# Kernel optimization log

Measured on AMD Instinct MI355X. Metric: run time of the kernel, lower is better.

## Reference

```python
import jax, jax.numpy as jnp
import numpy as np

N = 20000   # num_eeg_channels (graph nodes)
T = 512     # num_eeg_timesteps (GIN in_channels)
L = 256     # latent_features
HID = 512   # GIN hidden_channels
H = 4       # GATv2 heads
D = L // H  # per-head dim = 64
E = 320000  # edges


def setup_inputs() -> dict:
    key = jax.random.key(0)
    ks = jax.random.split(key, 16)
    s = 0.02
    f32 = jnp.float32
    return {
        "x": jax.random.normal(ks[0], (N, T), f32),
        "edge_index": jax.random.randint(ks[1], (2, E), 0, N, dtype=jnp.int64),
        "edge_attr": jax.random.normal(ks[2], (E,), f32),
        # GIN layer 1 MLP [T->HID->HID]
        "W1a": jax.random.normal(ks[3], (T, HID), f32) * s, "b1a": jnp.zeros((HID,), f32),
        "W1b": jax.random.normal(ks[4], (HID, HID), f32) * s, "b1b": jnp.zeros((HID,), f32),
        # GIN layer 2 MLP [HID->L->L]
        "W2a": jax.random.normal(ks[5], (HID, L), f32) * s, "b2a": jnp.zeros((L,), f32),
        "W2b": jax.random.normal(ks[6], (L, L), f32) * s, "b2b": jnp.zeros((L,), f32),
        # BatchNorm1d(L)
        "bn_g": jnp.ones((L,), f32), "bn_b": jnp.zeros((L,), f32),
        # GATv2Conv(L -> D, heads=H), separate src/dst projections, att vec, bias
        "Wl": jax.random.normal(ks[7], (L, H * D), f32) * s,
        "Wr": jax.random.normal(ks[8], (L, H * D), f32) * s,
        "att": jax.random.normal(ks[9], (H, D), f32) * s,
        "gat_b": jnp.zeros((H * D,), f32),
        # LayerNorm(N*L) and Linear(N*L, 1)
        "ln_g": jnp.ones((N * L,), f32), "ln_b": jnp.zeros((N * L,), f32),
        "Wp": jax.random.normal(ks[10], (N * L, 1), f32) * 0.001, "bp": jnp.zeros((1,), f32),
    }


def reference(x, edge_index, edge_attr, W1a, b1a, W1b, b1b, W2a, b2a, W2b, b2b,
              bn_g, bn_b, Wl, Wr, att, gat_b, ln_g, ln_b, Wp, bp):
    src, dst = edge_index[0], edge_index[1]

    # ---- GIN (2 layers; GINConv eps=0, edge_attr unused by GINConv) ----
    def gin_conv(h, Wa, ba, Wb, bb):
        agg = jax.ops.segment_sum(h[src], dst, num_segments=N)  # sum_{j->i} h_j
        z = h + agg
        return jax.nn.relu(z @ Wa + ba) @ Wb + bb

    h = jax.nn.relu(gin_conv(x, W1a, b1a, W1b, b1b))  # inter-layer ReLU
    h = gin_conv(h, W2a, b2a, W2b, b2b)               # [N, L]

    # ---- BatchNorm1d over node batch (training stats, biased var) ----
    mu = h.mean(axis=0)
    var = ((h - mu) ** 2).mean(axis=0)
    h = (h - mu) / jnp.sqrt(var + 1e-5) * bn_g + bn_b

    # ---- GATv2Conv (add_self_loops=False, eval so no attn dropout) ----
    xl = (h @ Wl).reshape(N, H, D)
    xr = (h @ Wr).reshape(N, H, D)
    e = jnp.einsum('ehd,hd->eh', jax.nn.leaky_relu(xl[src] + xr[dst], 0.2), att)  # [E,H]
    m = jax.ops.segment_max(e, dst, num_segments=N)          # per-target max
    ex = jnp.exp(e - m[dst])
    alpha = ex / jax.ops.segment_sum(ex, dst, num_segments=N)[dst]  # [E,H]
    gat_out = jax.ops.segment_sum(alpha[:, :, None] * xl[src], dst, num_segments=N)
    gat_out = gat_out.reshape(N, H * D) + gat_b              # [N, L]

    # ---- edge-attention scatter-add to nodes (faithful .view(4,-1)) ----
    edge_w = alpha.reshape(H, -1)                            # [H, E] (row-major, as torch .view)
    flat_idx = jnp.concatenate([src, dst])                   # each edge hits both endpoints
    vals = jnp.concatenate([edge_w, edge_w], axis=1)         # [H, 2E]
    node_att = jnp.zeros((H, N), e.dtype).at[:, flat_idx].add(vals)
    deg = jnp.bincount(edge_index.reshape(-1), length=N).astype(e.dtype)
    node_att = jax.nn.softmax(node_att / (deg + 1e-9)[None, :], axis=1)

    # ---- LayerNorm(N*L) + Linear + sigmoid ----
    feat = gat_out.reshape(1, N * L)
    fmu = feat.mean()
    fvar = ((feat - fmu) ** 2).mean()
    feat = (feat - fmu) / jnp.sqrt(fvar + 1e-5) * ln_g + ln_b
    pred = jax.nn.sigmoid(feat @ Wp + bp)                    # [1,1]

    return pred, node_att.mean(axis=0), edge_w.mean(axis=0)
```

## Files before the change

### kernel.cpp

```cpp
#include <hip/hip_runtime.h>
#include <hip/hip_bf16.h>

#define NN 20000
#define TT 512
#define LL 256
#define HH 4
#define DD 64
#define EE 320000

typedef __attribute__((ext_vector_type(8))) short short8;
typedef __attribute__((ext_vector_type(4))) float f32x4;

__device__ __forceinline__ float bf2f(unsigned short u) {
    return __uint_as_float((unsigned)u << 16);
}
__device__ __forceinline__ unsigned short f2bf(float f) {
    __hip_bfloat16 h = __float2bfloat16(f);
    unsigned short r;
    __builtin_memcpy(&r, &h, 2);
    return r;
}

__global__ void deg_kernel(const int* __restrict__ src, const int* __restrict__ dst,
                           int* deg_in, int* deg_tot) {
    int e = blockIdx.x * blockDim.x + threadIdx.x;
    if (e >= EE) return;
    atomicAdd(&deg_in[dst[e]], 1);
    atomicAdd(&deg_tot[src[e]], 1);
    atomicAdd(&deg_tot[dst[e]], 1);
}

__global__ void scan2_kernel(const int* __restrict__ deg0, int* rs0,
                             const int* __restrict__ deg1, int* rs1, int n) {
    __shared__ int sm[1024];
    __shared__ int s_carry;
    const int* deg = (blockIdx.x == 0) ? deg0 : deg1;
    int* row_start = (blockIdx.x == 0) ? rs0 : rs1;
    int tid = threadIdx.x;
    if (tid == 0) s_carry = 0;
    __syncthreads();
    for (int base = 0; base < n; base += 1024) {
        int i = base + tid;
        int v = (i < n) ? deg[i] : 0;
        sm[tid] = v;
        __syncthreads();
        for (int off = 1; off < 1024; off <<= 1) {
            int t = (tid >= off) ? sm[tid - off] : 0;
            __syncthreads();
            sm[tid] += t;
            __syncthreads();
        }
        int incl = sm[tid];
        int carry = s_carry;
        if (i < n) row_start[i] = carry + incl - v;
        __syncthreads();
        if (tid == 1023) s_carry = carry + sm[1023];
        __syncthreads();
    }
    if (tid == 0) row_start[n] = s_carry;
}

__global__ void fill_csr_kernel(const int* __restrict__ dst, const int* __restrict__ row_start,
                                int* cursor, int* csr) {
    int e = blockIdx.x * blockDim.x + threadIdx.x;
    if (e >= EE) return;
    int d = dst[e];
    int p = atomicAdd(&cursor[d], 1);
    csr[row_start[d] + p] = e;
}

__global__ void fill_adj2_kernel(const int* __restrict__ src, const int* __restrict__ dst,
                                 const int* __restrict__ rs2, int* cursor2, int* adj2) {
    int e = blockIdx.x * blockDim.x + threadIdx.x;
    if (e >= EE) return;
    int s = src[e];
    int p = atomicAdd(&cursor2[s], 1);
    adj2[rs2[s] + p] = e;
    int t = dst[e];
    int q = atomicAdd(&cursor2[t], 1);
    adj2[rs2[t] + q] = e;
}

__global__ void cast_bf_kernel(const float* __restrict__ in, unsigned short* __restrict__ out,
                               int n4) {
    int i = blockIdx.x * blockDim.x + threadIdx.x;
    if (i >= n4) return;
    float4 v = ((const float4*)in)[i];
    ushort4 o;
    o.x = f2bf(v.x); o.y = f2bf(v.y); o.z = f2bf(v.z); o.w = f2bf(v.w);
    ((ushort4*)out)[i] = o;
}

__global__ void wtrans_kernel(const float* __restrict__ W, unsigned short* __restrict__ Wt,
                              int K, int N) {
    __shared__ float t[32][33];
    int x = threadIdx.x & 31, y = threadIdx.x >> 5;
    int bn = blockIdx.x * 32, bk = blockIdx.y * 32;
#pragma unroll
    for (int i = 0; i < 32; i += 8) t[y + i][x] = W[(size_t)(bk + y + i) * N + bn + x];
    __syncthreads();
#pragma unroll
    for (int i = 0; i < 32; i += 8)
        Wt[(size_t)(bn + y + i) * K + bk + x] = f2bf(t[x][y + i]);
}

__global__ void agg_add_bf_kernel(const unsigned short* __restrict__ X,
                                  unsigned short* __restrict__ Z,
                                  const int* __restrict__ csr, const int* __restrict__ row_start,
                                  const int* __restrict__ src) {
    __shared__ int s_src[256];
    const int node = blockIdx.x, tid = threadIdx.x;
    const unsigned int* Xu = (const unsigned int*)X;
    const int start = row_start[node], end = row_start[node + 1];
    unsigned int self = Xu[(size_t)node * 256 + tid];
    float a0 = bf2f((unsigned short)(self & 0xffff));
    float a1 = bf2f((unsigned short)(self >> 16));
    for (int k0 = start; k0 < end; k0 += 256) {
        int k = k0 + tid;
        if (k < end) s_src[tid] = src[csr[k]];
        __syncthreads();
        int cnt = min(256, end - k0);
        for (int j = 0; j < cnt; ++j) {
            unsigned int v = Xu[(size_t)s_src[j] * 256 + tid];
            a0 += bf2f((unsigned short)(v & 0xffff));
            a1 += bf2f((unsigned short)(v >> 16));
        }
        __syncthreads();
    }
    ((unsigned int*)Z)[(size_t)node * 256 + tid] =
        (unsigned int)f2bf(a0) | ((unsigned int)f2bf(a1) << 16);
}

template <int RELU, int OUT_BF16>
__global__ __launch_bounds__(256)
void gemm_mfma_kernel(const unsigned short* __restrict__ A,
                      const unsigned short* __restrict__ Bt,
                      const float* __restrict__ bias, void* __restrict__ Cout,
                      int M, int K, int Nn) {
    __shared__ unsigned short lds[2][2][4][128][8];
    const int tid = threadIdx.x;
    const int wid = tid >> 6, lane = tid & 63;
    const int brow = blockIdx.y * 128, bcol = blockIdx.x * 128;
    const int wr = wid >> 1, wc = wid & 1;
    const int khi = lane >> 4, r15 = lane & 15;

    f32x4 acc[4][4] = {};

    const int q0 = wid * 2, q1 = wid * 2 + 1;
    const int kh0 = q0 >> 1, rh0 = q0 & 1;
    const int kh1 = q1 >> 1, rh1 = q1 & 1;
    int ar0 = brow + rh0 * 64 + lane; ar0 = ar0 < M ? ar0 : M - 1;
    int ar1 = brow + rh1 * 64 + lane; ar1 = ar1 < M ? ar1 : M - 1;
    const int bc0 = bcol + rh0 * 64 + lane;
    const int bc1 = bcol + rh1 * 64 + lane;
    const unsigned short* gA0 = A + (size_t)ar0 * K + kh0 * 8;
    const unsigned short* gA1 = A + (size_t)ar1 * K + kh1 * 8;
    const unsigned short* gB0 = Bt + (size_t)bc0 * K + kh0 * 8;
    const unsigned short* gB1 = Bt + (size_t)bc1 * K + kh1 * 8;

#define GLL(gp, lp) __builtin_amdgcn_global_load_lds( \
        (const __attribute__((address_space(1))) unsigned int*)(gp), \
        (__attribute__((address_space(3))) unsigned int*)(lp), 16, 0, 0)
#define STAGE(buf, kt) do { const int koff = (kt) * 32; \
        GLL(gA0 + koff, &lds[buf][0][kh0][rh0 * 64][0]); \
        GLL(gA1 + koff, &lds[buf][0][kh1][rh1 * 64][0]); \
        GLL(gB0 + koff, &lds[buf][1][kh0][rh0 * 64][0]); \
        GLL(gB1 + koff, &lds[buf][1][kh1][rh1 * 64][0]); \
    } while (0)

    const int NT = K >> 5;
    STAGE(0, 0);
    for (int kt = 0; kt < NT; ++kt) {
        const int cur = kt & 1;
        __syncthreads();
        if (kt + 1 < NT) STAGE(cur ^ 1, kt + 1);
        short8 af[4], bfv[4];
#pragma unroll
        for (int m = 0; m < 4; ++m)
            af[m] = *(const short8*)&lds[cur][0][khi][wr * 64 + m * 16 + r15][0];
#pragma unroll
        for (int n = 0; n < 4; ++n)
            bfv[n] = *(const short8*)&lds[cur][1][khi][wc * 64 + n * 16 + r15][0];
#pragma unroll
        for (int m = 0; m < 4; ++m)
#pragma unroll
            for (int n = 0; n < 4; ++n)
                acc[m][n] =
                    __builtin_amdgcn_mfma_f32_16x16x32_bf16(af[m], bfv[n], acc[m][n], 0, 0, 0);
    }
#undef STAGE
#undef GLL

#pragma unroll
    for (int m = 0; m < 4; ++m) {
#pragma unroll
        for (int n = 0; n < 4; ++n) {
            const int col = bcol + wc * 64 + n * 16 + r15;
            const float bb = bias ? bias[col] : 0.f;
            f32x4 v = acc[m][n];
#pragma unroll
            for (int r = 0; r < 4; ++r) {
                const int row = brow + wr * 64 + m * 16 + khi * 4 + r;
                if (row < M) {
                    float o = v[r] + bb;
                    if (RELU) o = fmaxf(o, 0.f);
                    if (OUT_BF16)
                        ((unsigned short*)Cout)[(size_t)row * Nn + col] = f2bf(o);
                    else
                        ((float*)Cout)[(size_t)row * Nn + col] = o;
                }
            }
        }
    }
}

__global__ void bn_stats_kernel(const float* __restrict__ h, float* cs, float* csq) {
    int col = threadIdx.x;
    int r0 = blockIdx.x * 100;
    int r1 = min(r0 + 100, NN);
    float s = 0.f, sq = 0.f;
    for (int r = r0; r < r1; r++) {
        float v = h[(size_t)r * 256 + col];
        s += v;
        sq += v * v;
    }
    atomicAdd(&cs[col], s);
    atomicAdd(&csq[col], sq);
}

__global__ void bn_apply_bf_kernel(const float* __restrict__ h, const float* __restrict__ cs,
                                   const float* __restrict__ csq, const float* __restrict__ g,
                                   const float* __restrict__ b, unsigned short* __restrict__ out) {
    int i = blockIdx.x * blockDim.x + threadIdx.x;
    if (i >= NN * 256) return;
    int col = i & 255;
    float mu = cs[col] * (1.f / NN);
    float var = csq[col] * (1.f / NN) - mu * mu;
    float inv = rsqrtf(var + 1e-5f);
    out[i] = f2bf((h[i] - mu) * inv * g[col] + b[col]);
}

__global__ void gat_fused_kernel(const unsigned short* __restrict__ xl,
                                 const unsigned short* __restrict__ xr,
                                 const int* __restrict__ csr, const int* __restrict__ rs,
                                 const int* __restrict__ src, const float* __restrict__ att,
                                 const float* __restrict__ gatb,
                                 float* __restrict__ alpha, float* __restrict__ out) {
    const int lane = threadIdx.x & 63;
    const int wave = threadIdx.x >> 6;
    const int node = blockIdx.x * 4 + wave;
    if (node >= NN) return;
    const int start = rs[node], end = rs[node + 1];
    const int deg = end - start;
    const int h = lane >> 4;
    const int l15 = lane & 15;

    const float4 attv = ((const float4*)att)[lane];
    const uint2 uxr = ((const uint2*)(xr + (size_t)node * 256))[lane];
    const float xr0 = bf2f((unsigned short)(uxr.x & 0xffff));
    const float xr1 = bf2f((unsigned short)(uxr.x >> 16));
    const float xr2 = bf2f((unsigned short)(uxr.y & 0xffff));
    const float xr3 = bf2f((unsigned short)(uxr.y >> 16));

    float m = -1e30f, S = 0.f;
    float O0 = 0.f, O1 = 0.f, O2 = 0.f, O3 = 0.f;
    float lg0 = 0.f, lg1 = 0.f, lg2 = 0.f, lg3 = 0.f;
    const bool fast = (deg <= 64);
    int eid = 0;

    for (int base = start; base < end; base += 64) {
        const int cnt = min(64, end - base);
        eid = (lane < cnt) ? csr[base + lane] : 0;
        int sid = (lane < cnt) ? src[eid] : 0;
        for (int i = 0; i < cnt; ++i) {
            const int s = __shfl(sid, i);
            const uint2 u = ((const uint2*)(xl + (size_t)s * 256))[lane];
            const float x0 = bf2f((unsigned short)(u.x & 0xffff));
            const float x1 = bf2f((unsigned short)(u.x >> 16));
            const float x2 = bf2f((unsigned short)(u.y & 0xffff));
            const float x3 = bf2f((unsigned short)(u.y >> 16));
            float a0 = x0 + xr0; a0 = a0 > 0.f ? a0 : 0.2f * a0;
            float a1 = x1 + xr1; a1 = a1 > 0.f ? a1 : 0.2f * a1;
            float a2 = x2 + xr2; a2 = a2 > 0.f ? a2 : 0.2f * a2;
            float a3 = x3 + xr3; a3 = a3 > 0.f ? a3 : 0.2f * a3;
            float p = a0 * attv.x + a1 * attv.y + a2 * attv.z + a3 * attv.w;
#pragma unroll
            for (int o = 1; o < 16; o <<= 1) p += __shfl_xor(p, o);
            if (fast && l15 == (i & 15)) {
                const int t = i >> 4;
                if (t == 0) lg0 = p;
                else if (t == 1) lg1 = p;
                else if (t == 2) lg2 = p;
                else lg3 = p;
            }
            const float mn = fmaxf(m, p);
            const float sc = __expf(m - mn);
            const float w = __expf(p - mn);
            S = S * sc + w;
            O0 = O0 * sc + w * x0;
            O1 = O1 * sc + w * x1;
            O2 = O2 * sc + w * x2;
            O3 = O3 * sc + w * x3;
            m = mn;
        }
    }

    const float rS = (deg > 0) ? 1.f / S : 0.f;
    const float4 bv = ((const float4*)gatb)[lane];
    float4 ov;
    ov.x = O0 * rS + bv.x; ov.y = O1 * rS + bv.y;
    ov.z = O2 * rS + bv.z; ov.w = O3 * rS + bv.w;
    ((float4*)(out + (size_t)node * 256))[lane] = ov;

    if (deg == 0) return;
    if (fast) {
#pragma unroll
        for (int t = 0; t < 4; ++t) {
            const int k = l15 + t * 16;
            if (k < deg) {
                const int e = __shfl(eid, k);
                const float l = (t == 0) ? lg0 : (t == 1) ? lg1 : (t == 2) ? lg2 : lg3;
                alpha[(size_t)e * 4 + h] = __expf(l - m) * rS;
            }
        }
    } else {
        for (int base = start; base < end; base += 64) {
            const int cnt = min(64, end - base);
            const int eid2 = (lane < cnt) ? csr[base + lane] : 0;
            const int sid2 = (lane < cnt) ? src[eid2] : 0;
            for (int i = 0; i < cnt; ++i) {
                const int s = __shfl(sid2, i);
                const uint2 u = ((const uint2*)(xl + (size_t)s * 256))[lane];
                float a0 = bf2f((unsigned short)(u.x & 0xffff)) + xr0; a0 = a0 > 0.f ? a0 : 0.2f * a0;
                float a1 = bf2f((unsigned short)(u.x >> 16)) + xr1;    a1 = a1 > 0.f ? a1 : 0.2f * a1;
                float a2 = bf2f((unsigned short)(u.y & 0xffff)) + xr2; a2 = a2 > 0.f ? a2 : 0.2f * a2;
                float a3 = bf2f((unsigned short)(u.y >> 16)) + xr3;    a3 = a3 > 0.f ? a3 : 0.2f * a3;
                float p = a0 * attv.x + a1 * attv.y + a2 * attv.z + a3 * attv.w;
#pragma unroll
                for (int o = 1; o < 16; o <<= 1) p += __shfl_xor(p, o);
                const int e = __shfl(eid2, i);
                if (l15 == 0) alpha[(size_t)e * 4 + h] = __expf(p - m) * rS;
            }
        }
    }
}

__global__ void node_att_gather_kernel(const float* __restrict__ abuf,
                                       const int* __restrict__ adj2,
                                       const int* __restrict__ rs2, float* __restrict__ na) {
    int lane = threadIdx.x & 63;
    int wave = threadIdx.x >> 6;
    int node = blockIdx.x * 4 + wave;
    if (node >= NN) return;
    int start = rs2[node], end = rs2[node + 1];
    float s0 = 0.f, s1 = 0.f, s2 = 0.f, s3 = 0.f;
    for (int k = start + lane; k < end; k += 64) {
        int e = adj2[k];
        s0 += abuf[e];
        s1 += abuf[EE + e];
        s2 += abuf[2 * EE + e];
        s3 += abuf[3 * EE + e];
    }
#pragma unroll
    for (int o = 32; o > 0; o >>= 1) {
        s0 += __shfl_xor(s0, o);
        s1 += __shfl_xor(s1, o);
        s2 += __shfl_xor(s2, o);
        s3 += __shfl_xor(s3, o);
    }
    if (lane == 0) {
        na[node] = s0;
        na[NN + node] = s1;
        na[2 * NN + node] = s2;
        na[3 * NN + node] = s3;
    }
}

__global__ void edge_mean_kernel(const float* __restrict__ abuf, float* __restrict__ out_edge) {
    int e = blockIdx.x * blockDim.x + threadIdx.x;
    if (e >= EE) return;
    out_edge[e] = 0.25f * (abuf[e] + abuf[EE + e] + abuf[2 * EE + e] + abuf[3 * EE + e]);
}

__global__ void head_stats_kernel(const float* __restrict__ na, const int* __restrict__ deg_tot,
                                  float* hm, float* hs) {
    __shared__ float red[1024];
    int h = blockIdx.x;
    int tid = threadIdx.x;
    float m = -1e30f;
    for (int i = tid; i < NN; i += 1024) {
        float v = na[h * NN + i] / ((float)deg_tot[i] + 1e-9f);
        m = fmaxf(m, v);
    }
    red[tid] = m;
    __syncthreads();
    for (int o = 512; o > 0; o >>= 1) {
        if (tid < o) red[tid] = fmaxf(red[tid], red[tid + o]);
        __syncthreads();
    }
    m = red[0];
    __syncthreads();
    float s = 0.f;
    for (int i = tid; i < NN; i += 1024) {
        float v = na[h * NN + i] / ((float)deg_tot[i] + 1e-9f);
        s += __expf(v - m);
    }
    red[tid] = s;
    __syncthreads();
    for (int o = 512; o > 0; o >>= 1) {
        if (tid < o) red[tid] += red[tid + o];
        __syncthreads();
    }
    if (tid == 0) {
        hm[h] = m;
        hs[h] = red[0];
    }
}

__global__ void node_out_kernel(const float* __restrict__ na, const int* __restrict__ deg_tot,
                                const float* __restrict__ hm, const float* __restrict__ hs,
                                float* __restrict__ out_node) {
    int i = blockIdx.x * blockDim.x + threadIdx.x;
    if (i >= NN) return;
    float acc = 0.f;
#pragma unroll
    for (int h = 0; h < 4; h++) {
        float v = na[h * NN + i] / ((float)deg_tot[i] + 1e-9f);
        acc += __expf(v - hm[h]) / hs[h];
    }
    out_node[i] = 0.25f * acc;
}

__global__ void ln_fused_kernel(const float* __restrict__ x, const float* __restrict__ g,
                                const float* __restrict__ b, const float* __restrict__ Wp,
                                float* __restrict__ part) {
    const int total4 = NN * 64;
    const float4* x4 = (const float4*)x;
    const float4* g4 = (const float4*)g;
    const float4* b4 = (const float4*)b;
    const float4* w4 = (const float4*)Wp;
    float s1 = 0.f, s2 = 0.f, s3 = 0.f, s4 = 0.f, s5 = 0.f;
    for (int i = blockIdx.x * blockDim.x + threadIdx.x; i < total4;
         i += gridDim.x * blockDim.x) {
        float4 xv = x4[i], gv = g4[i], bv = b4[i], wv = w4[i];
        s1 += xv.x + xv.y + xv.z + xv.w;
        s2 += xv.x * xv.x + xv.y * xv.y + xv.z * xv.z + xv.w * xv.w;
        float gw0 = gv.x * wv.x, gw1 = gv.y * wv.y, gw2 = gv.z * wv.z, gw3 = gv.w * wv.w;
        s3 += xv.x * gw0 + xv.y * gw1 + xv.z * gw2 + xv.w * gw3;
        s4 += gw0 + gw1 + gw2 + gw3;
        s5 += bv.x * wv.x + bv.y * wv.y + bv.z * wv.z + bv.w * wv.w;
    }
#pragma unroll
    for (int o = 32; o > 0; o >>= 1) {
        s1 += __shfl_xor(s1, o);
        s2 += __shfl_xor(s2, o);
        s3 += __shfl_xor(s3, o);
        s4 += __shfl_xor(s4, o);
        s5 += __shfl_xor(s5, o);
    }
    __shared__ float sm[4][5];
    int lane = threadIdx.x & 63, wv_ = threadIdx.x >> 6;
    if (lane == 0) {
        sm[wv_][0] = s1; sm[wv_][1] = s2; sm[wv_][2] = s3; sm[wv_][3] = s4; sm[wv_][4] = s5;
    }
    __syncthreads();
    if (threadIdx.x == 0) {
        float t1 = 0.f, t2 = 0.f, t3 = 0.f, t4 = 0.f, t5 = 0.f;
#pragma unroll
        for (int w = 0; w < 4; ++w) {
            t1 += sm[w][0]; t2 += sm[w][1]; t3 += sm[w][2]; t4 += sm[w][3]; t5 += sm[w][4];
        }
        part[0 * 512 + blockIdx.x] = t1;
        part[1 * 512 + blockIdx.x] = t2;
        part[2 * 512 + blockIdx.x] = t3;
        part[3 * 512 + blockIdx.x] = t4;
        part[4 * 512 + blockIdx.x] = t5;
    }
}

__global__ void ln_final_kernel(const float* __restrict__ part, const float* __restrict__ bp,
                                float* __restrict__ out) {
    float v0 = part[0 * 512 + threadIdx.x];
    float v1 = part[1 * 512 + threadIdx.x];
    float v2 = part[2 * 512 + threadIdx.x];
    float v3 = part[3 * 512 + threadIdx.x];
    float v4 = part[4 * 512 + threadIdx.x];
#pragma unroll
    for (int o = 32; o > 0; o >>= 1) {
        v0 += __shfl_xor(v0, o);
        v1 += __shfl_xor(v1, o);
        v2 += __shfl_xor(v2, o);
        v3 += __shfl_xor(v3, o);
        v4 += __shfl_xor(v4, o);
    }
    __shared__ float sm[8][5];
    int lane = threadIdx.x & 63, wv_ = threadIdx.x >> 6;
    if (lane == 0) {
        sm[wv_][0] = v0; sm[wv_][1] = v1; sm[wv_][2] = v2; sm[wv_][3] = v3; sm[wv_][4] = v4;
    }
    __syncthreads();
    if (threadIdx.x == 0) {
        float S1 = 0.f, S2 = 0.f, S3 = 0.f, S4 = 0.f, S5 = 0.f;
#pragma unroll
        for (int w = 0; w < 8; ++w) {
            S1 += sm[w][0]; S2 += sm[w][1]; S3 += sm[w][2]; S4 += sm[w][3]; S5 += sm[w][4];
        }
        const float M = (float)NN * 256.f;
        float mu = S1 / M;
        float var = S2 / M - mu * mu;
        float inv = rsqrtf(var + 1e-5f);
        float z = inv * (S3 - mu * S4) + S5 + bp[0];
        out[0] = 1.f / (1.f + __expf(-z));
    }
}

extern "C" void kernel_launch(void* const* d_in, const int* in_sizes, int n_in,
                              void* d_out, int out_size, void* d_ws, size_t ws_size,
                              hipStream_t stream) {
    const float* x    = (const float*)d_in[0];
    const int* ei     = (const int*)d_in[1];
    const float* W1a  = (const float*)d_in[3];
    const float* b1a  = (const float*)d_in[4];
    const float* W1b  = (const float*)d_in[5];
    const float* b1b  = (const float*)d_in[6];
    const float* W2a  = (const float*)d_in[7];
    const float* b2a  = (const float*)d_in[8];
    const float* W2b  = (const float*)d_in[9];
    const float* b2b  = (const float*)d_in[10];
    const float* bn_g = (const float*)d_in[11];
    const float* bn_b = (const float*)d_in[12];
    const float* Wl   = (const float*)d_in[13];
    const float* Wr   = (const float*)d_in[14];
    const float* att  = (const float*)d_in[15];
    const float* gatb = (const float*)d_in[16];
    const float* ln_g = (const float*)d_in[17];
    const float* ln_b = (const float*)d_in[18];
    const float* Wp   = (const float*)d_in[19];
    const float* bp   = (const float*)d_in[20];

    const int* src = ei;
    const int* dst = ei + EE;

    float* out = (float*)d_out;
    float* out_pred = out;
    float* out_node = out + 1;
    float* out_edge = out + 1 + NN;

    unsigned short* B0 = (unsigned short*)d_ws;
    unsigned short* B1 = B0 + (size_t)NN * 512;
    unsigned short* B2 = B1 + (size_t)NN * 512;
    unsigned short* B3 = B2 + (size_t)NN * 512;
    float* hbuf = (float*)B0;
    unsigned short* xl = B1;
    unsigned short* xr = B3;
    float* gout = (float*)B0;

    unsigned short* W1at = B3 + (size_t)NN * 512;
    unsigned short* W1bt = W1at + 512 * 512;
    unsigned short* W2at = W1bt + 512 * 512;
    unsigned short* W2bt = W2at + 256 * 512;
    unsigned short* Wlt  = W2bt + 256 * 256;
    unsigned short* Wrt  = Wlt + 256 * 256;
    float* alpha = (float*)(Wrt + 256 * 256);
    float* na    = alpha + (size_t)EE * 4;
    float* csum  = na + 4 * NN;
    float* csq_  = csum + 256;
    float* hm    = csq_ + 256;
    float* hs    = hm + 4;
    float* part  = hs + 4;
    int* deg_in     = (int*)(part + 5 * 512);
    int* deg_tot    = deg_in + NN;
    int* row_start  = deg_tot + NN;
    int* row_start2 = row_start + NN + 1;
    int* cursor     = row_start2 + NN + 1;
    int* cursor2    = cursor + NN;
    int* csr        = cursor2 + NN;
    int* adj2       = csr + EE;

    hipMemsetAsync(csum, 0, (size_t)(256 + 256 + 4 + 4) * sizeof(float), stream);
    hipMemsetAsync(deg_in, 0, (size_t)(6 * NN + 2) * sizeof(int), stream);

    const int EB = (EE + 255) / 256;

    wtrans_kernel<<<dim3(16, 16), 256, 0, stream>>>(W1a, W1at, 512, 512);
    wtrans_kernel<<<dim3(16, 16), 256, 0, stream>>>(W1b, W1bt, 512, 512);
    wtrans_kernel<<<dim3(8, 16), 256, 0, stream>>>(W2a, W2at, 512, 256);
    wtrans_kernel<<<dim3(8, 8), 256, 0, stream>>>(W2b, W2bt, 256, 256);
    wtrans_kernel<<<dim3(8, 8), 256, 0, stream>>>(Wl, Wlt, 256, 256);
    wtrans_kernel<<<dim3(8, 8), 256, 0, stream>>>(Wr, Wrt, 256, 256);

    cast_bf_kernel<<<(NN * 512 / 4 + 255) / 256, 256, 0, stream>>>(x, B0, NN * 512 / 4);

    deg_kernel<<<EB, 256, 0, stream>>>(src, dst, deg_in, deg_tot);
    scan2_kernel<<<2, 1024, 0, stream>>>(deg_in, row_start, deg_tot, row_start2, NN);
    fill_csr_kernel<<<EB, 256, 0, stream>>>(dst, row_start, cursor, csr);
    fill_adj2_kernel<<<EB, 256, 0, stream>>>(src, dst, row_start2, cursor2, adj2);

    agg_add_bf_kernel<<<NN, 256, 0, stream>>>(B0, B1, csr, row_start, src);
    gemm_mfma_kernel<1, 1><<<dim3(4, 157), 256, 0, stream>>>(B1, W1at, b1a, B2, NN, 512, 512);
    gemm_mfma_kernel<1, 1><<<dim3(4, 157), 256, 0, stream>>>(B2, W1bt, b1b, B3, NN, 512, 512);
    agg_add_bf_kernel<<<NN, 256, 0, stream>>>(B3, B0, csr, row_start, src);
    gemm_mfma_kernel<1, 1><<<dim3(2, 157), 256, 0, stream>>>(B0, W2at, b2a, B1, NN, 512, 256);
    gemm_mfma_kernel<0, 0><<<dim3(2, 157), 256, 0, stream>>>(B1, W2bt, b2b, hbuf, NN, 256, 256);

    bn_stats_kernel<<<200, 256, 0, stream>>>(hbuf, csum, csq_);
    bn_apply_bf_kernel<<<(NN * 256 + 255) / 256, 256, 0, stream>>>(hbuf, csum, csq_, bn_g, bn_b,
                                                                   B2);

    gemm_mfma_kernel<0, 1><<<dim3(2, 157), 256, 0, stream>>>(B2, Wlt, nullptr, xl, NN, 256, 256);
    gemm_mfma_kernel<0, 1><<<dim3(2, 157), 256, 0, stream>>>(B2, Wrt, nullptr, xr, NN, 256, 256);

    gat_fused_kernel<<<(NN + 3) / 4, 256, 0, stream>>>(xl, xr, csr, row_start, src, att, gatb,
                                                       alpha, gout);

    node_att_gather_kernel<<<NN / 4, 256, 0, stream>>>(alpha, adj2, row_start2, na);
    edge_mean_kernel<<<EB, 256, 0, stream>>>(alpha, out_edge);
    head_stats_kernel<<<4, 1024, 0, stream>>>(na, deg_tot, hm, hs);
    node_out_kernel<<<(NN + 255) / 256, 256, 0, stream>>>(na, deg_tot, hm, hs, out_node);

    ln_fused_kernel<<<512, 256, 0, stream>>>(gout, ln_g, ln_b, Wp, part);
    ln_final_kernel<<<1, 512, 0, stream>>>(part, bp, out_pred);
}
```

Before: 703.2 us.

## Reorder GIN layer 2 to project before aggregating, use wave-per-node gather

```diff
diff --git a/kernel.cpp b/kernel.cpp
--- a/kernel.cpp
+++ b/kernel.cpp
@@ -19,6 +19,13 @@
     unsigned short r;
     __builtin_memcpy(&r, &h, 2);
     return r;
+}
+__device__ __forceinline__ void acc2(float& a0, float& a1, unsigned int u) {
+    a0 += __uint_as_float(u << 16);
+    a1 += __uint_as_float(u & 0xffff0000u);
+}
+__device__ __forceinline__ unsigned int pack2(float a0, float a1) {
+    return (unsigned int)f2bf(a0) | ((unsigned int)f2bf(a1) << 16);
 }
 
 __global__ void deg_kernel(const int* __restrict__ src, const int* __restrict__ dst,
@@ -30,34 +37,61 @@
     atomicAdd(&deg_tot[dst[e]], 1);
 }
 
-__global__ void scan2_kernel(const int* __restrict__ deg0, int* rs0,
-                             const int* __restrict__ deg1, int* rs1, int n) {
+#define SCHUNKS 20
+__global__ void scan_partial_kernel(const int* __restrict__ deg0, const int* __restrict__ deg1,
+                                    int* __restrict__ psum) {
+    __shared__ int red[4];
+    int j = blockIdx.x;
+    const int* deg = (j < SCHUNKS) ? deg0 : deg1;
+    int c = (j < SCHUNKS) ? j : j - SCHUNKS;
+    int base = c * 1024;
+    int s = 0;
+#pragma unroll
+    for (int t = 0; t < 4; ++t) {
+        int i = base + threadIdx.x + t * 256;
+        if (i < NN) s += deg[i];
+    }
+#pragma unroll
+    for (int o = 32; o > 0; o >>= 1) s += __shfl_xor(s, o);
+    int lane = threadIdx.x & 63, wv = threadIdx.x >> 6;
+    if (lane == 0) red[wv] = s;
+    __syncthreads();
+    if (threadIdx.x == 0) psum[j] = red[0] + red[1] + red[2] + red[3];
+}
+
+__global__ void scan_offsets_kernel(const int* __restrict__ psum, int* __restrict__ coff,
+                                    int* rs0, int* rs1) {
+    int a = threadIdx.x;
+    if (a >= 2) return;
+    int run = 0;
+    for (int c = 0; c < SCHUNKS; ++c) {
+        coff[a * SCHUNKS + c] = run;
+        run += psum[a * SCHUNKS + c];
+    }
+    if (a == 0) rs0[NN] = run;
+    else rs1[NN] = run;
+}
+
+__global__ void scan_apply_kernel(const int* __restrict__ deg0, const int* __restrict__ deg1,
+                                  const int* __restrict__ coff, int* __restrict__ rs0,
+                                  int* __restrict__ rs1) {
     __shared__ int sm[1024];
-    __shared__ int s_carry;
-    const int* deg = (blockIdx.x == 0) ? deg0 : deg1;
-    int* row_start = (blockIdx.x == 0) ? rs0 : rs1;
+    int j = blockIdx.x;
+    const int* deg = (j < SCHUNKS) ? deg0 : deg1;
+    int* rs = (j < SCHUNKS) ? rs0 : rs1;
+    int c = (j < SCHUNKS) ? j : j - SCHUNKS;
     int tid = threadIdx.x;
-    if (tid == 0) s_carry = 0;
-    __syncthreads();
-    for (int base = 0; base < n; base += 1024) {
-        int i = base + tid;
-        int v = (i < n) ? deg[i] : 0;
-        sm[tid] = v;
+    int i = c * 1024 + tid;
+    int v = (i < NN) ? deg[i] : 0;
+    sm[tid] = v;
+    __syncthreads();
+    for (int off = 1; off < 1024; off <<= 1) {
+        int t = (tid >= off) ? sm[tid - off] : 0;
         __syncthreads();
-        for (int off = 1; off < 1024; off <<= 1) {
-            int t = (tid >= off) ? sm[tid - off] : 0;
-            __syncthreads();
-            sm[tid] += t;
-            __syncthreads();
-        }
-        int incl = sm[tid];
-        int carry = s_carry;
-        if (i < n) row_start[i] = carry + incl - v;
+        sm[tid] += t;
         __syncthreads();
-        if (tid == 1023) s_carry = carry + sm[1023];
-        __syncthreads();
-    }
-    if (tid == 0) row_start[n] = s_carry;
+    }
+    if (i < NN) rs[i] = coff[j] + sm[tid] - v;
 }
 
 __global__ void fill_csr_kernel(const int* __restrict__ dst, const int* __restrict__ row_start,
@@ -91,11 +125,23 @@
     ((ushort4*)out)[i] = o;
 }
 
-__global__ void wtrans_kernel(const float* __restrict__ W, unsigned short* __restrict__ Wt,
-                              int K, int N) {
+__global__ void wtrans_all_kernel(const float* __restrict__ W1a, const float* __restrict__ W1b,
+                                  const float* __restrict__ W2a, const float* __restrict__ W2b,
+                                  const float* __restrict__ Wl, const float* __restrict__ Wr,
+                                  unsigned short* W1at, unsigned short* W1bt,
+                                  unsigned short* W2at, unsigned short* W2bt,
+                                  unsigned short* Wlt, unsigned short* Wrt) {
     __shared__ float t[32][33];
+    int j = blockIdx.x;
+    const float* W; unsigned short* Wt; int K, N, tx;
+    if (j < 256)      { W = W1a; Wt = W1at; K = 512; N = 512; tx = 16; }
+    else if (j < 512) { W = W1b; Wt = W1bt; K = 512; N = 512; tx = 16; j -= 256; }
+    else if (j < 640) { W = W2a; Wt = W2at; K = 512; N = 256; tx = 8;  j -= 512; }
+    else if (j < 704) { W = W2b; Wt = W2bt; K = 256; N = 256; tx = 8;  j -= 640; }
+    else if (j < 768) { W = Wl;  Wt = Wlt;  K = 256; N = 256; tx = 8;  j -= 704; }
+    else              { W = Wr;  Wt = Wrt;  K = 256; N = 256; tx = 8;  j -= 768; }
+    int bn = (j % tx) * 32, bk = (j / tx) * 32;
     int x = threadIdx.x & 31, y = threadIdx.x >> 5;
-    int bn = blockIdx.x * 32, bk = blockIdx.y * 32;
 #pragma unroll
     for (int i = 0; i < 32; i += 8) t[y + i][x] = W[(size_t)(bk + y + i) * N + bn + x];
     __syncthreads();
@@ -104,31 +150,59 @@
         Wt[(size_t)(bn + y + i) * K + bk + x] = f2bf(t[x][y + i]);
 }
 
-__global__ void agg_add_bf_kernel(const unsigned short* __restrict__ X,
-                                  unsigned short* __restrict__ Z,
-                                  const int* __restrict__ csr, const int* __restrict__ row_start,
-                                  const int* __restrict__ src) {
-    __shared__ int s_src[256];
-    const int node = blockIdx.x, tid = threadIdx.x;
-    const unsigned int* Xu = (const unsigned int*)X;
-    const int start = row_start[node], end = row_start[node + 1];
-    unsigned int self = Xu[(size_t)node * 256 + tid];
-    float a0 = bf2f((unsigned short)(self & 0xffff));
-    float a1 = bf2f((unsigned short)(self >> 16));
-    for (int k0 = start; k0 < end; k0 += 256) {
-        int k = k0 + tid;
-        if (k < end) s_src[tid] = src[csr[k]];
-        __syncthreads();
-        int cnt = min(256, end - k0);
-        for (int j = 0; j < cnt; ++j) {
-            unsigned int v = Xu[(size_t)s_src[j] * 256 + tid];
-            a0 += bf2f((unsigned short)(v & 0xffff));
-            a1 += bf2f((unsigned short)(v >> 16));
+template <int ELEMS, int BIAS_RELU>
+__global__ void agg_wave_kernel(const unsigned short* __restrict__ X,
+                                unsigned short* __restrict__ Z,
+                                const int* __restrict__ csr, const int* __restrict__ rs,
+                                const int* __restrict__ src, const float* __restrict__ bias) {
+    const int lane = threadIdx.x & 63;
+    const int wave = threadIdx.x >> 6;
+    const int node = blockIdx.x * 4 + wave;
+    if (node >= NN) return;
+    const int F = ELEMS * 64;
+    const int start = rs[node], end = rs[node + 1];
+    float a[ELEMS];
+    if constexpr (ELEMS == 8) {
+        uint4 u = ((const uint4*)(X + (size_t)node * F))[lane];
+        a[0] = __uint_as_float(u.x << 16); a[1] = __uint_as_float(u.x & 0xffff0000u);
+        a[2] = __uint_as_float(u.y << 16); a[3] = __uint_as_float(u.y & 0xffff0000u);
+        a[4] = __uint_as_float(u.z << 16); a[5] = __uint_as_float(u.z & 0xffff0000u);
+        a[6] = __uint_as_float(u.w << 16); a[7] = __uint_as_float(u.w & 0xffff0000u);
+    } else {
+        uint2 u = ((const uint2*)(X + (size_t)node * F))[lane];
+        a[0] = __uint_as_float(u.x << 16); a[1] = __uint_as_float(u.x & 0xffff0000u);
+        a[2] = __uint_as_float(u.y << 16); a[3] = __uint_as_float(u.y & 0xffff0000u);
+    }
+    for (int base = start; base < end; base += 64) {
+        const int cnt = min(64, end - base);
+        int e = (lane < cnt) ? csr[base + lane] : 0;
+        int sid = (lane < cnt) ? src[e] : 0;
+        for (int i = 0; i < cnt; ++i) {
+            const int s = __shfl(sid, i);
+            if constexpr (ELEMS == 8) {
+                uint4 u = ((const uint4*)(X + (size_t)s * F))[lane];
+                acc2(a[0], a[1], u.x); acc2(a[2], a[3], u.y);
+                acc2(a[4], a[5], u.z); acc2(a[6], a[7], u.w);
+            } else {
+                uint2 u = ((const uint2*)(X + (size_t)s * F))[lane];
+                acc2(a[0], a[1], u.x); acc2(a[2], a[3], u.y);
+            }
         }
-        __syncthreads();
-    }
-    ((unsigned int*)Z)[(size_t)node * 256 + tid] =
-        (unsigned int)f2bf(a0) | ((unsigned int)f2bf(a1) << 16);
+    }
+    if (BIAS_RELU) {
+#pragma unroll
+        for (int j = 0; j < ELEMS; ++j) a[j] = fmaxf(a[j] + bias[lane * ELEMS + j], 0.f);
+    }
+    if constexpr (ELEMS == 8) {
+        uint4 o;
+        o.x = pack2(a[0], a[1]); o.y = pack2(a[2], a[3]);
+        o.z = pack2(a[4], a[5]); o.w = pack2(a[6], a[7]);
+        ((uint4*)(Z + (size_t)node * F))[lane] = o;
+    } else {
+        uint2 o;
+        o.x = pack2(a[0], a[1]); o.y = pack2(a[2], a[3]);
+        ((uint2*)(Z + (size_t)node * F))[lane] = o;
+    }
 }
 
 template <int RELU, int OUT_BF16>
@@ -576,32 +650,32 @@
     int* cursor2    = cursor + NN;
     int* csr        = cursor2 + NN;
     int* adj2       = csr + EE;
+    int* psum       = adj2 + 2 * EE;
+    int* coff       = psum + 40;
 
     hipMemsetAsync(csum, 0, (size_t)(256 + 256 + 4 + 4) * sizeof(float), stream);
     hipMemsetAsync(deg_in, 0, (size_t)(6 * NN + 2) * sizeof(int), stream);
 
     const int EB = (EE + 255) / 256;
 
-    wtrans_kernel<<<dim3(16, 16), 256, 0, stream>>>(W1a, W1at, 512, 512);
-    wtrans_kernel<<<dim3(16, 16), 256, 0, stream>>>(W1b, W1bt, 512, 512);
-    wtrans_kernel<<<dim3(8, 16), 256, 0, stream>>>(W2a, W2at, 512, 256);
-    wtrans_kernel<<<dim3(8, 8), 256, 0, stream>>>(W2b, W2bt, 256, 256);
-    wtrans_kernel<<<dim3(8, 8), 256, 0, stream>>>(Wl, Wlt, 256, 256);
-    wtrans_kernel<<<dim3(8, 8), 256, 0, stream>>>(Wr, Wrt, 256, 256);
-
+    wtrans_all_kernel<<<832, 256, 0, stream>>>(W1a, W1b, W2a, W2b, Wl, Wr, W1at, W1bt, W2at,
+                                               W2bt, Wlt, Wrt);
     cast_bf_kernel<<<(NN * 512 / 4 + 255) / 256, 256, 0, stream>>>(x, B0, NN * 512 / 4);
 
     deg_kernel<<<EB, 256, 0, stream>>>(src, dst, deg_in, deg_tot);
-    scan2_kernel<<<2, 1024, 0, stream>>>(deg_in, row_start, deg_tot, row_start2, NN);
+    scan_partial_kernel<<<2 * SCHUNKS, 256, 0, stream>>>(deg_in, deg_tot, psum);
+    scan_offsets_kernel<<<1, 64, 0, stream>>>(psum, coff, row_start, row_start2);
+    scan_apply_kernel<<<2 * SCHUNKS, 1024, 0, stream>>>(deg_in, deg_tot, coff, row_start,
+                                                        row_start2);
     fill_csr_kernel<<<EB, 256, 0, stream>>>(dst, row_start, cursor, csr);
     fill_adj2_kernel<<<EB, 256, 0, stream>>>(src, dst, row_start2, cursor2, adj2);
 
-    agg_add_bf_kernel<<<NN, 256, 0, stream>>>(B0, B1, csr, row_start, src);
+    agg_wave_kernel<8, 0><<<NN / 4, 256, 0, stream>>>(B0, B1, csr, row_start, src, nullptr);
     gemm_mfma_kernel<1, 1><<<dim3(4, 157), 256, 0, stream>>>(B1, W1at, b1a, B2, NN, 512, 512);
     gemm_mfma_kernel<1, 1><<<dim3(4, 157), 256, 0, stream>>>(B2, W1bt, b1b, B3, NN, 512, 512);
-    agg_add_bf_kernel<<<NN, 256, 0, stream>>>(B3, B0, csr, row_start, src);
-    gemm_mfma_kernel<1, 1><<<dim3(2, 157), 256, 0, stream>>>(B0, W2at, b2a, B1, NN, 512, 256);
-    gemm_mfma_kernel<0, 0><<<dim3(2, 157), 256, 0, stream>>>(B1, W2bt, b2b, hbuf, NN, 256, 256);
+    gemm_mfma_kernel<0, 1><<<dim3(2, 157), 256, 0, stream>>>(B3, W2at, nullptr, B1, NN, 512, 256);
+    agg_wave_kernel<4, 1><<<NN / 4, 256, 0, stream>>>(B1, B2, csr, row_start, src, b2a);
+    gemm_mfma_kernel<0, 0><<<dim3(2, 157), 256, 0, stream>>>(B2, W2bt, b2b, hbuf, NN, 256, 256);
 
     bn_stats_kernel<<<200, 256, 0, stream>>>(hbuf, csum, csq_);
     bn_apply_bf_kernel<<<(NN * 256 + 255) / 256, 256, 0, stream>>>(hbuf, csum, csq_, bn_g, bn_b,
```

After: 643.9 us. 1.09x faster.
